# Optimization experiments

Hardware: AMD Instinct MI355X
Metric: run time of the kernel (lower is better)

The kernel has to match this reference:

```python
import jax, jax.numpy as jnp
import numpy as np

K = 16  # neighbors, matches init k


def _knn_indices(points, k):
    # points: (N, 3) -> idx: (N, k), self excluded
    sq = jnp.sum(points ** 2, axis=-1, keepdims=True)          # (N, 1)
    dist2 = sq + sq.T - 2.0 * (points @ points.T)              # (N, N)
    dist2 = jnp.clip(dist2, 0.0)
    n = points.shape[0]
    diag = jnp.eye(n, dtype=bool)
    dist2 = jnp.where(diag, jnp.inf, dist2)
    _, idx = jax.lax.top_k(-dist2, k)                          # smallest k
    return idx


def _features_single(xyz, normals, k):
    # xyz, normals: (N, 3)
    idx = _knn_indices(xyz, k)                                 # (N, k)
    neighbors = xyz[idx]                                       # (N, k, 3)
    centroid = neighbors.mean(axis=1, keepdims=True)           # (N, 1, 3)
    centered = neighbors - centroid                            # (N, k, 3)
    cov = jnp.einsum('nki,nkj->nij', centered, centered) / max(k - 1, 1)  # (N, 3, 3)
    w, v = jnp.linalg.eigh(cov.astype(jnp.float32))            # ascending
    w = w[:, ::-1].astype(xyz.dtype)                           # descending (N, 3)
    v = v[:, :, ::-1].astype(xyz.dtype)                        # (N, 3, 3)
    pca_normal = v[:, :, 2]                                    # smallest-variance dir
    dot = jnp.sum(pca_normal * normals, axis=-1, keepdims=True)
    pca_normal = pca_normal * jnp.sign(dot)
    consistency = jnp.abs(dot)                                 # (N, 1)
    total_var = jnp.clip(w.sum(axis=-1, keepdims=True), 1e-8)
    curvature = w[:, 2:3] / total_var                          # (N, 1)
    perp = jnp.abs(jnp.sum(centered * pca_normal[:, None, :], axis=-1))  # (N, k)
    roughness = perp.mean(axis=-1, keepdims=True)              # (N, 1)
    return jnp.concatenate([consistency, normals, curvature, roughness], axis=-1)


def setup_inputs() -> dict:
    key = jax.random.key(0)
    k1, k2 = jax.random.split(key)
    B, N = 2, 12288
    xyz = jax.random.normal(k1, (B, N, 3), dtype=jnp.float32)
    nrm = jax.random.normal(k2, (B, N, 3), dtype=jnp.float32)
    nrm = nrm / jnp.linalg.norm(nrm, axis=-1, keepdims=True)   # unit normals
    return {"xyz": xyz, "normals": nrm}


def reference(xyz, normals):
    return jax.vmap(lambda p, n: _features_single(p, n, K))(xyz, normals)
```

## Files before the change

### kernel.cpp

```cpp
#include <hip/hip_runtime.h>


#define NPTS 12288
#define NBATCH 2
#define NQ (NPTS * NBATCH)
#define KNN 16
#define NCH 16
#define CHSZ (NPTS / NCH)
#define MKEEP 8
#define QBLK (NQ / 256)

typedef unsigned long long u64;
typedef unsigned short u16;
typedef unsigned int u32;

#define SWAPU(a, b) { u32 _lo = min(a, b); u32 _hi = max(a, b); a = _lo; b = _hi; }
#define SWAP64(a, b) { u64 _lo = (a) < (b) ? (a) : (b); u64 _hi = (a) < (b) ? (b) : (a); a = _lo; b = _hi; }
#define MIN64(a, b) ((a) < (b) ? (a) : (b))
#define DIST(dst, px, py, pz) { float _dx = Qx - (px); float _dy = Qy - (py); float _dz = Qz - (pz); \
                                dst = fmaf(_dz, _dz, fmaf(_dy, _dy, _dx * _dx)); }
#define KEY(kk, dd, rel) { kk = (__float_as_uint(dd) & 0xFFFFFC00u) | (u32)(rel); }

__global__ __launch_bounds__(256) void pack_kernel(const float* __restrict__ xyz,
                                                   float* __restrict__ xs,
                                                   float* __restrict__ ys,
                                                   float* __restrict__ zs,
                                                   float4* __restrict__ pts4) {
  int i = blockIdx.x * 256 + threadIdx.x;
  if (i < NQ) {
    float x = xyz[3 * i + 0], y = xyz[3 * i + 1], z = xyz[3 * i + 2];
    xs[i] = x; ys[i] = y; zs[i] = z;
    pts4[i] = make_float4(x, y, z, fmaf(z, z, fmaf(y, y, x * x)));
  }
}

__global__ __launch_bounds__(256) void knn_kernel(const float4* __restrict__ pts4,
                                                  u16* __restrict__ cidx) {
  int bid = blockIdx.x;
  int qb = bid % QBLK;
  int chk = bid / QBLK;
  int q0 = qb * 256;
  int b = q0 / NPTS;
  int base = b * NPTS + chk * CHSZ;
  int q = q0 + threadIdx.x;

  float4 Q = pts4[q];
  float qq = Q.w;
  float m2x = -2.0f * Q.x, m2y = -2.0f * Q.y, m2z = -2.0f * Q.z;

  const float4* cp = pts4 + base;

  u32 r0 = ~0u, r1 = ~0u, r2 = ~0u, r3 = ~0u, r4 = ~0u, r5 = ~0u, r6 = ~0u, r7 = ~0u;

#define SVAL(dst, c) dst = fmaf(m2x, (c).x, fmaf(m2y, (c).y, fmaf(m2z, (c).z, qq + (c).w)));

  float4 a0 = cp[0], a1 = cp[1], a2 = cp[2], a3 = cp[3];
  float4 a4 = cp[4], a5 = cp[5], a6 = cp[6], a7 = cp[7];

#pragma unroll 1
  for (int c0 = 0; c0 < CHSZ; c0 += 8) {
    float4 n0 = cp[c0 + 8], n1 = cp[c0 + 9], n2 = cp[c0 + 10], n3 = cp[c0 + 11];
    float4 n4 = cp[c0 + 12], n5 = cp[c0 + 13], n6 = cp[c0 + 14], n7 = cp[c0 + 15];

    float e0, e1, e2, e3, e4, e5, e6, e7;
    SVAL(e0, a0) SVAL(e1, a1) SVAL(e2, a2) SVAL(e3, a3)
    SVAL(e4, a4) SVAL(e5, a5) SVAL(e6, a6) SVAL(e7, a7)
    u32 d0, d1, d2, d3, d4, d5, d6, d7;
    KEY(d0, e0, c0 + 0); KEY(d1, e1, c0 + 1); KEY(d2, e2, c0 + 2); KEY(d3, e3, c0 + 3);
    KEY(d4, e4, c0 + 4); KEY(d5, e5, c0 + 5); KEY(d6, e6, c0 + 6); KEY(d7, e7, c0 + 7);
    SWAPU(d0, d1) SWAPU(d2, d3) SWAPU(d4, d5) SWAPU(d6, d7)
    SWAPU(d0, d2) SWAPU(d1, d3) SWAPU(d4, d6) SWAPU(d5, d7)
    SWAPU(d1, d2) SWAPU(d5, d6)
    SWAPU(d0, d4) SWAPU(d1, d5) SWAPU(d2, d6) SWAPU(d3, d7)
    SWAPU(d2, d4) SWAPU(d3, d5)
    SWAPU(d1, d2) SWAPU(d3, d4) SWAPU(d5, d6)
    u32 m0 = min(r0, d7), m1 = min(r1, d6), m2 = min(r2, d5), m3 = min(r3, d4);
    u32 m4 = min(r4, d3), m5 = min(r5, d2), m6 = min(r6, d1), m7 = min(r7, d0);
    SWAPU(m0, m4) SWAPU(m1, m5) SWAPU(m2, m6) SWAPU(m3, m7)
    SWAPU(m0, m2) SWAPU(m1, m3) SWAPU(m4, m6) SWAPU(m5, m7)
    SWAPU(m0, m1) SWAPU(m2, m3) SWAPU(m4, m5) SWAPU(m6, m7)
    r0 = m0; r1 = m1; r2 = m2; r3 = m3; r4 = m4; r5 = m5; r6 = m6; r7 = m7;

    a0 = n0; a1 = n1; a2 = n2; a3 = n3; a4 = n4; a5 = n5; a6 = n6; a7 = n7;
  }
#undef SVAL

  u32 cb = (u32)(chk * CHSZ);
  uint4 w;
  w.x = (cb + (r0 & 1023u)) | ((cb + (r1 & 1023u)) << 16);
  w.y = (cb + (r2 & 1023u)) | ((cb + (r3 & 1023u)) << 16);
  w.z = (cb + (r4 & 1023u)) | ((cb + (r5 & 1023u)) << 16);
  w.w = (cb + (r6 & 1023u)) | ((cb + (r7 & 1023u)) << 16);
  *(uint4*)(cidx + (size_t)q * (NCH * MKEEP) + chk * MKEEP) = w;
}

__global__ __launch_bounds__(256) void feat_kernel(const float* __restrict__ xs,
                                                   const float* __restrict__ ys,
                                                   const float* __restrict__ zs,
                                                   const float* __restrict__ normals,
                                                   const u16* __restrict__ cidx,
                                                   float* __restrict__ out) {
  int t = blockIdx.x * 256 + threadIdx.x;
  int b = t / NPTS;
  int qi = t - b * NPTS;
  int bbase = b * NPTS;

  float Qx = xs[t], Qy = ys[t], Qz = zs[t];

  const uint4* crow = (const uint4*)(cidx + (size_t)t * (NCH * MKEEP));

  u64 run[KNN];
#pragma unroll
  for (int i = 0; i < KNN; ++i) run[i] = ~0ULL;

#pragma unroll 1
  for (int ch = 0; ch < NCH; ++ch) {
    uint4 w = crow[ch];
    int ix[8];
    ix[0] = (int)(w.x & 0xFFFFu); ix[1] = (int)(w.x >> 16);
    ix[2] = (int)(w.y & 0xFFFFu); ix[3] = (int)(w.y >> 16);
    ix[4] = (int)(w.z & 0xFFFFu); ix[5] = (int)(w.z >> 16);
    ix[6] = (int)(w.w & 0xFFFFu); ix[7] = (int)(w.w >> 16);
    u64 s0, s1, s2, s3, s4, s5, s6, s7;
#define MK(sv, j) { int _i = ix[j]; float _d; DIST(_d, xs[bbase + _i], ys[bbase + _i], zs[bbase + _i]); \
                    sv = ((u64)__float_as_uint(_d) << 32) | (u32)_i; if (_i == qi) sv = ~0ULL; }
    MK(s0, 0) MK(s1, 1) MK(s2, 2) MK(s3, 3) MK(s4, 4) MK(s5, 5) MK(s6, 6) MK(s7, 7)
#undef MK
    SWAP64(s0, s1) SWAP64(s2, s3) SWAP64(s4, s5) SWAP64(s6, s7)
    SWAP64(s0, s2) SWAP64(s1, s3) SWAP64(s4, s6) SWAP64(s5, s7)
    SWAP64(s1, s2) SWAP64(s5, s6)
    SWAP64(s0, s4) SWAP64(s1, s5) SWAP64(s2, s6) SWAP64(s3, s7)
    SWAP64(s2, s4) SWAP64(s3, s5)
    SWAP64(s1, s2) SWAP64(s3, s4) SWAP64(s5, s6)
    run[8]  = MIN64(run[8],  s7);
    run[9]  = MIN64(run[9],  s6);
    run[10] = MIN64(run[10], s5);
    run[11] = MIN64(run[11], s4);
    run[12] = MIN64(run[12], s3);
    run[13] = MIN64(run[13], s2);
    run[14] = MIN64(run[14], s1);
    run[15] = MIN64(run[15], s0);
#pragma unroll
    for (int j = 8; j >= 1; j >>= 1) {
#pragma unroll
      for (int i = 0; i < KNN; ++i) {
        if ((i & j) == 0) { SWAP64(run[i], run[i | j]) }
      }
    }
  }

  float nx[KNN], ny[KNN], nz[KNN];
  float sx = 0.f, sy = 0.f, sz = 0.f;
#pragma unroll
  for (int i = 0; i < KNN; ++i) {
    int ni = (int)(u32)run[i];
    float px = xs[bbase + ni], py = ys[bbase + ni], pz = zs[bbase + ni];
    nx[i] = px; ny[i] = py; nz[i] = pz;
    sx += px; sy += py; sz += pz;
  }
  const float invK = 1.0f / 16.0f;
  float cx = sx * invK, cy = sy * invK, cz = sz * invK;

  float c00 = 0.f, c01 = 0.f, c02 = 0.f, c11 = 0.f, c12 = 0.f, c22 = 0.f;
#pragma unroll
  for (int i = 0; i < KNN; ++i) {
    float dx = nx[i] - cx, dy = ny[i] - cy, dz = nz[i] - cz;
    c00 += dx * dx; c01 += dx * dy; c02 += dx * dz;
    c11 += dy * dy; c12 += dy * dz; c22 += dz * dz;
  }
  const float inv15 = 1.0f / 15.0f;
  c00 *= inv15; c01 *= inv15; c02 *= inv15;
  c11 *= inv15; c12 *= inv15; c22 *= inv15;

  double a00 = c00, a01 = c01, a02 = c02, a11 = c11, a12 = c12, a22 = c22;
  double tr = a00 + a11 + a22;
  double qm = tr * (1.0 / 3.0);
  double p1 = a01 * a01 + a02 * a02 + a12 * a12;
  double b00 = a00 - qm, b11 = a11 - qm, b22 = a22 - qm;
  double p2 = b00 * b00 + b11 * b11 + b22 * b22 + 2.0 * p1;
  double lmin = qm;
  if (p2 > 0.0) {
    double p = sqrt(p2 * (1.0 / 6.0));
    double ip = 1.0 / p;
    double q00 = b00 * ip, q01 = a01 * ip, q02 = a02 * ip;
    double q11 = b11 * ip, q12 = a12 * ip, q22 = b22 * ip;
    double det = q00 * (q11 * q22 - q12 * q12) - q01 * (q01 * q22 - q12 * q02) +
                 q02 * (q01 * q12 - q11 * q02);
    double r = 0.5 * det;
    r = r < -1.0 ? -1.0 : (r > 1.0 ? 1.0 : r);
    double phi = acos(r) * (1.0 / 3.0);
    lmin = qm + 2.0 * p * cos(phi + 2.0943951023931953);
  }

  double m00 = a00 - lmin, m11 = a11 - lmin, m22 = a22 - lmin;
  double v0x = a01 * a12 - a02 * m11;
  double v0y = a02 * a01 - m00 * a12;
  double v0z = m00 * m11 - a01 * a01;
  double v1x = a01 * m22 - a02 * a12;
  double v1y = a02 * a02 - m00 * m22;
  double v1z = m00 * a12 - a01 * a02;
  double v2x = m11 * m22 - a12 * a12;
  double v2y = a12 * a02 - a01 * m22;
  double v2z = a01 * a12 - m11 * a02;
  double n0 = v0x * v0x + v0y * v0y + v0z * v0z;
  double n1 = v1x * v1x + v1y * v1y + v1z * v1z;
  double n2 = v2x * v2x + v2y * v2y + v2z * v2z;
  double vx, vy, vz, nn;
  if (n0 >= n1 && n0 >= n2) { vx = v0x; vy = v0y; vz = v0z; nn = n0; }
  else if (n1 >= n2)        { vx = v1x; vy = v1y; vz = v1z; nn = n1; }
  else                      { vx = v2x; vy = v2y; vz = v2z; nn = n2; }
  if (nn < 1e-60) { vx = 0.0; vy = 0.0; vz = 1.0; nn = 1.0; }
  double inn = 1.0 / sqrt(nn);
  float vxf = (float)(vx * inn), vyf = (float)(vy * inn), vzf = (float)(vz * inn);

  float s = 0.f;
#pragma unroll
  for (int i = 0; i < KNN; ++i) {
    s += fabsf((nx[i] - cx) * vxf + (ny[i] - cy) * vyf + (nz[i] - cz) * vzf);
  }

  float nrx = normals[3 * (size_t)t + 0];
  float nry = normals[3 * (size_t)t + 1];
  float nrz = normals[3 * (size_t)t + 2];
  float dot = vxf * nrx + vyf * nry + vzf * nrz;
  float cons = fabsf(dot);
  float trf = c00 + c11 + c22;
  float curv = (float)lmin / fmaxf(trf, 1e-8f);
  float* o = out + (size_t)t * 6;
  o[0] = cons;
  o[1] = nrx;
  o[2] = nry;
  o[3] = nrz;
  o[4] = curv;
  o[5] = s * invK;
}

extern "C" void kernel_launch(void* const* d_in, const int* in_sizes, int n_in,
                              void* d_out, int out_size, void* d_ws, size_t ws_size,
                              hipStream_t stream) {
  const float* xyz = (const float*)d_in[0];
  const float* normals = (const float*)d_in[1];
  float* out = (float*)d_out;

  float* xs = (float*)d_ws;
  float* ys = xs + NQ;
  float* zs = ys + NQ;
  float4* pts4 = (float4*)(zs + NQ);
  u16* cidx = (u16*)(pts4 + NQ + 8);

  pack_kernel<<<NQ / 256, 256, 0, stream>>>(xyz, xs, ys, zs, pts4);
  knn_kernel<<<QBLK * NCH, 256, 0, stream>>>(pts4, cidx);
  feat_kernel<<<NQ / 256, 256, 0, stream>>>(xs, ys, zs, normals, cidx, out);
}
```

Measured before the change: 145.7 us.

## Stage candidate chunk in LDS and process four queries per thread in kNN

The kNN kernel now loads each candidate chunk once into shared memory as SoA arrays and has each thread handle four queries, so every candidate load is reused four times instead of being re-fetched from global memory per query. The packed float4 buffer is replaced by separate x/y/z and squared-norm arrays. The feature kernel's block size drops to 64 threads to spread work over more blocks. The trade-off is higher register pressure from four running top-8 lists per thread, and fewer kNN blocks in flight.

```diff
diff --git a/kernel.cpp b/kernel.cpp
--- a/kernel.cpp
+++ b/kernel.cpp
@@ -8,7 +8,9 @@
 #define NCH 16
 #define CHSZ (NPTS / NCH)
 #define MKEEP 8
-#define QBLK (NQ / 256)
+#define RQ 4
+#define QGRP (256 * RQ)
+#define NQB (NQ / QGRP)
 
 typedef unsigned long long u64;
 typedef unsigned short u16;
@@ -25,82 +27,127 @@
                                                    float* __restrict__ xs,
                                                    float* __restrict__ ys,
                                                    float* __restrict__ zs,
-                                                   float4* __restrict__ pts4) {
+                                                   float* __restrict__ ps) {
   int i = blockIdx.x * 256 + threadIdx.x;
   if (i < NQ) {
     float x = xyz[3 * i + 0], y = xyz[3 * i + 1], z = xyz[3 * i + 2];
     xs[i] = x; ys[i] = y; zs[i] = z;
-    pts4[i] = make_float4(x, y, z, fmaf(z, z, fmaf(y, y, x * x)));
+    ps[i] = fmaf(z, z, fmaf(y, y, x * x));
   }
 }
 
-__global__ __launch_bounds__(256) void knn_kernel(const float4* __restrict__ pts4,
-                                                  u16* __restrict__ cidx) {
+__global__ __launch_bounds__(256, 2) void knn_kernel(const float* __restrict__ xs,
+                                                     const float* __restrict__ ys,
+                                                     const float* __restrict__ zs,
+                                                     const float* __restrict__ ps,
+                                                     u16* __restrict__ cidx) {
   int bid = blockIdx.x;
-  int qb = bid % QBLK;
-  int chk = bid / QBLK;
-  int q0 = qb * 256;
-  int b = q0 / NPTS;
+  int qb = bid % NQB;
+  int chk = bid / NQB;
+  int qbase = qb * QGRP;
+  int b = qbase / NPTS;
   int base = b * NPTS + chk * CHSZ;
-  int q = q0 + threadIdx.x;
-
-  float4 Q = pts4[q];
-  float qq = Q.w;
-  float m2x = -2.0f * Q.x, m2y = -2.0f * Q.y, m2z = -2.0f * Q.z;
-
-  const float4* cp = pts4 + base;
-
-  u32 r0 = ~0u, r1 = ~0u, r2 = ~0u, r3 = ~0u, r4 = ~0u, r5 = ~0u, r6 = ~0u, r7 = ~0u;
-
-#define SVAL(dst, c) dst = fmaf(m2x, (c).x, fmaf(m2y, (c).y, fmaf(m2z, (c).z, qq + (c).w)));
-
-  float4 a0 = cp[0], a1 = cp[1], a2 = cp[2], a3 = cp[3];
-  float4 a4 = cp[4], a5 = cp[5], a6 = cp[6], a7 = cp[7];
+
+  __shared__ __align__(16) float lx[CHSZ];
+  __shared__ __align__(16) float ly[CHSZ];
+  __shared__ __align__(16) float lz[CHSZ];
+  __shared__ __align__(16) float lp[CHSZ];
+  {
+    float4* sx = (float4*)lx; float4* sy = (float4*)ly;
+    float4* sz = (float4*)lz; float4* sp = (float4*)lp;
+    const float4* gx = (const float4*)(xs + base);
+    const float4* gy = (const float4*)(ys + base);
+    const float4* gz = (const float4*)(zs + base);
+    const float4* gp = (const float4*)(ps + base);
+    if (threadIdx.x < CHSZ / 4) {
+      sx[threadIdx.x] = gx[threadIdx.x];
+      sy[threadIdx.x] = gy[threadIdx.x];
+      sz[threadIdx.x] = gz[threadIdx.x];
+      sp[threadIdx.x] = gp[threadIdx.x];
+    }
+  }
+  __syncthreads();
+
+  float m2x[RQ], m2y[RQ], m2z[RQ], qq[RQ];
+#pragma unroll
+  for (int k = 0; k < RQ; ++k) {
+    int q = qbase + k * 256 + threadIdx.x;
+    m2x[k] = -2.0f * xs[q];
+    m2y[k] = -2.0f * ys[q];
+    m2z[k] = -2.0f * zs[q];
+    qq[k] = ps[q];
+  }
+
+  u32 run[RQ][8];
+#pragma unroll
+  for (int k = 0; k < RQ; ++k)
+#pragma unroll
+    for (int j = 0; j < 8; ++j) run[k][j] = ~0u;
+
+  const float4* lx4 = (const float4*)lx;
+  const float4* ly4 = (const float4*)ly;
+  const float4* lz4 = (const float4*)lz;
+  const float4* lp4 = (const float4*)lp;
 
 #pragma unroll 1
   for (int c0 = 0; c0 < CHSZ; c0 += 8) {
-    float4 n0 = cp[c0 + 8], n1 = cp[c0 + 9], n2 = cp[c0 + 10], n3 = cp[c0 + 11];
-    float4 n4 = cp[c0 + 12], n5 = cp[c0 + 13], n6 = cp[c0 + 14], n7 = cp[c0 + 15];
-
-    float e0, e1, e2, e3, e4, e5, e6, e7;
-    SVAL(e0, a0) SVAL(e1, a1) SVAL(e2, a2) SVAL(e3, a3)
-    SVAL(e4, a4) SVAL(e5, a5) SVAL(e6, a6) SVAL(e7, a7)
-    u32 d0, d1, d2, d3, d4, d5, d6, d7;
-    KEY(d0, e0, c0 + 0); KEY(d1, e1, c0 + 1); KEY(d2, e2, c0 + 2); KEY(d3, e3, c0 + 3);
-    KEY(d4, e4, c0 + 4); KEY(d5, e5, c0 + 5); KEY(d6, e6, c0 + 6); KEY(d7, e7, c0 + 7);
-    SWAPU(d0, d1) SWAPU(d2, d3) SWAPU(d4, d5) SWAPU(d6, d7)
-    SWAPU(d0, d2) SWAPU(d1, d3) SWAPU(d4, d6) SWAPU(d5, d7)
-    SWAPU(d1, d2) SWAPU(d5, d6)
-    SWAPU(d0, d4) SWAPU(d1, d5) SWAPU(d2, d6) SWAPU(d3, d7)
-    SWAPU(d2, d4) SWAPU(d3, d5)
-    SWAPU(d1, d2) SWAPU(d3, d4) SWAPU(d5, d6)
-    u32 m0 = min(r0, d7), m1 = min(r1, d6), m2 = min(r2, d5), m3 = min(r3, d4);
-    u32 m4 = min(r4, d3), m5 = min(r5, d2), m6 = min(r6, d1), m7 = min(r7, d0);
-    SWAPU(m0, m4) SWAPU(m1, m5) SWAPU(m2, m6) SWAPU(m3, m7)
-    SWAPU(m0, m2) SWAPU(m1, m3) SWAPU(m4, m6) SWAPU(m5, m7)
-    SWAPU(m0, m1) SWAPU(m2, m3) SWAPU(m4, m5) SWAPU(m6, m7)
-    r0 = m0; r1 = m1; r2 = m2; r3 = m3; r4 = m4; r5 = m5; r6 = m6; r7 = m7;
-
-    a0 = n0; a1 = n1; a2 = n2; a3 = n3; a4 = n4; a5 = n5; a6 = n6; a7 = n7;
-  }
+    int i4 = c0 >> 2;
+    float4 xA = lx4[i4], xB = lx4[i4 + 1];
+    float4 yA = ly4[i4], yB = ly4[i4 + 1];
+    float4 zA = lz4[i4], zB = lz4[i4 + 1];
+    float4 pA = lp4[i4], pB = lp4[i4 + 1];
+
+#pragma unroll
+    for (int k = 0; k < RQ; ++k) {
+      float M2X = m2x[k], M2Y = m2y[k], M2Z = m2z[k], QQ = qq[k];
+#define SVAL(dst, px, py, pz, pp) dst = fmaf(M2X, (px), fmaf(M2Y, (py), fmaf(M2Z, (pz), QQ + (pp))));
+      float e0, e1, e2, e3, e4, e5, e6, e7;
+      SVAL(e0, xA.x, yA.x, zA.x, pA.x) SVAL(e1, xA.y, yA.y, zA.y, pA.y)
+      SVAL(e2, xA.z, yA.z, zA.z, pA.z) SVAL(e3, xA.w, yA.w, zA.w, pA.w)
+      SVAL(e4, xB.x, yB.x, zB.x, pB.x) SVAL(e5, xB.y, yB.y, zB.y, pB.y)
+      SVAL(e6, xB.z, yB.z, zB.z, pB.z) SVAL(e7, xB.w, yB.w, zB.w, pB.w)
 #undef SVAL
+      u32 d0, d1, d2, d3, d4, d5, d6, d7;
+      KEY(d0, e0, c0 + 0); KEY(d1, e1, c0 + 1); KEY(d2, e2, c0 + 2); KEY(d3, e3, c0 + 3);
+      KEY(d4, e4, c0 + 4); KEY(d5, e5, c0 + 5); KEY(d6, e6, c0 + 6); KEY(d7, e7, c0 + 7);
+      SWAPU(d0, d1) SWAPU(d2, d3) SWAPU(d4, d5) SWAPU(d6, d7)
+      SWAPU(d0, d2) SWAPU(d1, d3) SWAPU(d4, d6) SWAPU(d5, d7)
+      SWAPU(d1, d2) SWAPU(d5, d6)
+      SWAPU(d0, d4) SWAPU(d1, d5) SWAPU(d2, d6) SWAPU(d3, d7)
+      SWAPU(d2, d4) SWAPU(d3, d5)
+      SWAPU(d1, d2) SWAPU(d3, d4) SWAPU(d5, d6)
+      u32 m0 = min(run[k][0], d7), m1 = min(run[k][1], d6);
+      u32 m2 = min(run[k][2], d5), m3 = min(run[k][3], d4);
+      u32 m4 = min(run[k][4], d3), m5 = min(run[k][5], d2);
+      u32 m6 = min(run[k][6], d1), m7 = min(run[k][7], d0);
+      SWAPU(m0, m4) SWAPU(m1, m5) SWAPU(m2, m6) SWAPU(m3, m7)
+      SWAPU(m0, m2) SWAPU(m1, m3) SWAPU(m4, m6) SWAPU(m5, m7)
+      SWAPU(m0, m1) SWAPU(m2, m3) SWAPU(m4, m5) SWAPU(m6, m7)
+      run[k][0] = m0; run[k][1] = m1; run[k][2] = m2; run[k][3] = m3;
+      run[k][4] = m4; run[k][5] = m5; run[k][6] = m6; run[k][7] = m7;
+    }
+  }
 
   u32 cb = (u32)(chk * CHSZ);
-  uint4 w;
-  w.x = (cb + (r0 & 1023u)) | ((cb + (r1 & 1023u)) << 16);
-  w.y = (cb + (r2 & 1023u)) | ((cb + (r3 & 1023u)) << 16);
-  w.z = (cb + (r4 & 1023u)) | ((cb + (r5 & 1023u)) << 16);
-  w.w = (cb + (r6 & 1023u)) | ((cb + (r7 & 1023u)) << 16);
-  *(uint4*)(cidx + (size_t)q * (NCH * MKEEP) + chk * MKEEP) = w;
+#pragma unroll
+  for (int k = 0; k < RQ; ++k) {
+    int q = qbase + k * 256 + threadIdx.x;
+    uint4 w;
+    w.x = (cb + (run[k][0] & 1023u)) | ((cb + (run[k][1] & 1023u)) << 16);
+    w.y = (cb + (run[k][2] & 1023u)) | ((cb + (run[k][3] & 1023u)) << 16);
+    w.z = (cb + (run[k][4] & 1023u)) | ((cb + (run[k][5] & 1023u)) << 16);
+    w.w = (cb + (run[k][6] & 1023u)) | ((cb + (run[k][7] & 1023u)) << 16);
+    *(uint4*)(cidx + (size_t)q * (NCH * MKEEP) + chk * MKEEP) = w;
+  }
 }
 
-__global__ __launch_bounds__(256) void feat_kernel(const float* __restrict__ xs,
-                                                   const float* __restrict__ ys,
-                                                   const float* __restrict__ zs,
-                                                   const float* __restrict__ normals,
-                                                   const u16* __restrict__ cidx,
-                                                   float* __restrict__ out) {
-  int t = blockIdx.x * 256 + threadIdx.x;
+__global__ __launch_bounds__(64) void feat_kernel(const float* __restrict__ xs,
+                                                  const float* __restrict__ ys,
+                                                  const float* __restrict__ zs,
+                                                  const float* __restrict__ normals,
+                                                  const u16* __restrict__ cidx,
+                                                  float* __restrict__ out) {
+  int t = blockIdx.x * 64 + threadIdx.x;
   int b = t / NPTS;
   int qi = t - b * NPTS;
   int bbase = b * NPTS;
@@ -245,10 +292,10 @@
   float* xs = (float*)d_ws;
   float* ys = xs + NQ;
   float* zs = ys + NQ;
-  float4* pts4 = (float4*)(zs + NQ);
-  u16* cidx = (u16*)(pts4 + NQ + 8);
-
-  pack_kernel<<<NQ / 256, 256, 0, stream>>>(xyz, xs, ys, zs, pts4);
-  knn_kernel<<<QBLK * NCH, 256, 0, stream>>>(pts4, cidx);
-  feat_kernel<<<NQ / 256, 256, 0, stream>>>(xs, ys, zs, normals, cidx, out);
+  float* ps = zs + NQ;
+  u16* cidx = (u16*)(ps + NQ);
+
+  pack_kernel<<<NQ / 256, 256, 0, stream>>>(xyz, xs, ys, zs, ps);
+  knn_kernel<<<NQB * NCH, 256, 0, stream>>>(xs, ys, zs, ps, cidx);
+  feat_kernel<<<NQ / 64, 64, 0, stream>>>(xs, ys, zs, normals, cidx, out);
 }
```

After: 163.6 us. 1.12x slower.
